# Optimization experiments

Measured on AMD Instinct MI355X. Metric: run time of the kernel, lower is better.

The kernel has to match this reference:

```python
import jax, jax.numpy as jnp
import numpy as np


def conv1x1(x, w, b):
    # x: [B,Cin,H,W], w: [Cout,Cin], b: [Cout]
    return jnp.einsum('bchw,oc->bohw', x, w) + b[None, :, None, None]


def setup_inputs() -> dict:
    key = jax.random.key(0)
    ks = jax.random.split(key, 10)
    B, Cm, C, H, W = 4, 6, 64, 64, 64
    map1 = jax.random.normal(ks[0], (B, Cm, H, W), jnp.float32)
    map2 = jax.random.normal(ks[1], (B, Cm, H, W), jnp.float32)
    feature_map = jax.random.normal(ks[2], (B, C, H, W), jnp.float32)
    # 1x1 conv params (kaiming-ish scale)
    wb = jax.random.normal(ks[3], (Cm, Cm), jnp.float32) / np.sqrt(Cm)
    bb = jnp.zeros((Cm,), jnp.float32)
    wc = jax.random.normal(ks[4], (Cm, Cm), jnp.float32) / np.sqrt(Cm)
    bc = jnp.zeros((Cm,), jnp.float32)
    wd = jax.random.normal(ks[5], (C, C), jnp.float32) / np.sqrt(C)
    bd = jnp.zeros((C,), jnp.float32)
    alpha = jnp.zeros((1,), jnp.float32)
    return {"map1": map1, "map2": map2, "feature_map": feature_map,
            "wb": wb, "bb": bb, "wc": wc, "bc": bc, "wd": wd, "bd": bd,
            "alpha": alpha}


def reference(map1, map2, feature_map, wb, bb, wc, bc, wd, bd, alpha):
    B, _, H, W = map1.shape
    N = H * W
    # conv1x1 projections, flatten spatial
    feat_b = conv1x1(map1, wb, bb).reshape(B, -1, N).transpose(0, 2, 1)  # [B,N,6]
    feat_c = conv1x1(map2, wc, bc).reshape(B, -1, N)                      # [B,6,N]
    attention_s = jax.nn.softmax(jnp.einsum('bnc,bcm->bnm', feat_b, feat_c), axis=-1)  # [B,N,N]
    feat_d = conv1x1(feature_map, wd, bd).reshape(B, -1, N)               # [B,C,N]
    # bmm with attention_s^T: out[b,c,n] = sum_m feat_d[b,c,m] * attn[b,n,m]
    feat_e = jnp.einsum('bcm,bnm->bcn', feat_d, attention_s).reshape(B, -1, H, W)
    return alpha * feat_e + feature_map
```

## Files before the change

### kernel.cpp

```cpp
#include <hip/hip_runtime.h>
#include <hip/hip_bf16.h>
#include <math.h>


#define BATCH 4
#define CMAP  6
#define CH    64
#define NSP   4096
#define TN    64
#define NTH   32
#define PSTR  72

typedef __attribute__((ext_vector_type(8))) short short8;
typedef __attribute__((ext_vector_type(4))) float f32x4;

#if __has_builtin(__builtin_amdgcn_exp2f)
#define EXP2(x) __builtin_amdgcn_exp2f(x)
#else
#define EXP2(x) exp2f(x)
#endif

__device__ __forceinline__ unsigned f2bf(float f) {
    unsigned u = __float_as_uint(f);
    return (u + 0x7fffu + ((u >> 16) & 1u)) >> 16;
}

#define INVLN2 1.44269504088896f
#define SHIFT_BF16 0xC238u
#define ONE_BF16   0x3F80u


__global__ void proj_kernel(const float* __restrict__ map1, const float* __restrict__ map2,
                            const float* __restrict__ fm,
                            const float* __restrict__ wb, const float* __restrict__ bb,
                            const float* __restrict__ wc, const float* __restrict__ bc,
                            const float* __restrict__ wd, const float* __restrict__ bd,
                            unsigned short* __restrict__ featq8,
                            unsigned short* __restrict__ featk8,
                            unsigned short* __restrict__ featdf)
{
    __shared__ unsigned short vfrag[2048];

    const int b    = blockIdx.z;
    const int half = blockIdx.y;
    const int lane = threadIdx.x & 63;
    const int og   = threadIdx.x >> 6;
    const int n    = blockIdx.x * 64 + lane;

    const int ht = lane >> 5;
    const int mm = lane & 31;
    const int q4 = mm >> 3, jj = mm & 7;
    const int cb_local = og >> 1;
    float vals[CH];
#pragma unroll
    for (int c = 0; c < CH; ++c)
        vals[c] = fm[(size_t)(b*CH + c)*NSP + n];
#pragma unroll
    for (int oi = 0; oi < 8; ++oi) {
        const int o = half*32 + og*8 + oi;
        float a = bd[o];
#pragma unroll
        for (int c = 0; c < CH; ++c)
            a = fmaf(vals[c], wd[o*CH + c], a);
        const int r = (og & 1)*8 + oi;
        vfrag[(ht*2 + cb_local)*512 + (q4*16 + r)*8 + jj] = (unsigned short)f2bf(a);
    }

    if (half == 0 && og == 0) {
        float v1[CMAP], v2[CMAP];
#pragma unroll
        for (int c = 0; c < CMAP; ++c) {
            v1[c] = map1[(size_t)(b*CMAP + c)*NSP + n];
            v2[c] = map2[(size_t)(b*CMAP + c)*NSP + n];
        }
        unsigned qv[CMAP], kv[CMAP];
#pragma unroll
        for (int o = 0; o < CMAP; ++o) {
            float a1 = bb[o], a2 = bc[o];
#pragma unroll
            for (int c = 0; c < CMAP; ++c) {
                a1 = fmaf(v1[c], wb[o*CMAP + c], a1);
                a2 = fmaf(v2[c], wc[o*CMAP + c], a2);
            }
            qv[o] = f2bf(a1 * INVLN2);
            kv[o] = f2bf(a2);
        }
        uint4 qw, kw;
        qw.x = qv[0] | (qv[1] << 16);
        qw.y = qv[2] | (qv[3] << 16);
        qw.z = qv[4] | (qv[5] << 16);
        qw.w = SHIFT_BF16;
        kw.x = kv[0] | (kv[1] << 16);
        kw.y = kv[2] | (kv[3] << 16);
        kw.z = kv[4] | (kv[5] << 16);
        kw.w = ONE_BF16;
        *(uint4*)&featq8[(size_t)(b*NSP + n)*8] = qw;
        *(uint4*)&featk8[(size_t)(b*NSP + n)*8] = kw;
    }

    __syncthreads();

    {
        const int tt = threadIdx.x;
        const uint4 d = *(const uint4*)&vfrag[tt*8];
        const int ht2 = tt >> 7, inner = tt & 127;
        const size_t off = (((size_t)(b*128 + blockIdx.x*2 + ht2)*4) + half*2)*512
                         + (size_t)inner*8;
        *(uint4*)&featdf[off] = d;
    }
}

__global__ __launch_bounds__(256, 2)
void attn_kernel(const unsigned short* __restrict__ featq8,
                 const unsigned short* __restrict__ featk8,
                 const unsigned short* __restrict__ featdf,
                 const float* __restrict__ fm, const float* __restrict__ alpha_p,
                 float* __restrict__ out)
{
    __shared__ unsigned short p_scr[2][4][16*PSTR];
    __shared__ float cmb[2][64][21];

    const int b    = blockIdx.y;
    const int t    = threadIdx.x;
    const int lane = t & 63, w = t >> 6;
    const int row16 = lane & 15, quad = lane >> 4;
    const int qsub  = w >> 1;
    const int khalf = w & 1;
    const int n0w  = blockIdx.x * 32 + qsub * 16;
    const int m0   = khalf * (NSP/2);

    short8 qf = {0,0,0,0,0,0,0,0};
    if (quad == 0)
        qf = *(const short8*)&featq8[(size_t)(b*NSP + n0w + row16)*8];

    const short8 onesb = {(short)ONE_BF16,(short)ONE_BF16,(short)ONE_BF16,(short)ONE_BF16,
                          (short)ONE_BF16,(short)ONE_BF16,(short)ONE_BF16,(short)ONE_BF16};

    const unsigned short* kbase = featk8 + ((size_t)(b*NSP + m0) + row16)*8 + quad*8;
    const unsigned short* vfb = featdf + ((size_t)b*128*4)*512 + lane*8;
    const int hb = khalf * 64;

    const f32x4 zf = {0.f,0.f,0.f,0.f};
    f32x4 acc[4] = {zf, zf, zf, zf};
    f32x4 accL = zf;
    const int prow = row16 * PSTR;

#define PAM_DO(pwp, mb, sv)                                                     \
    {                                                                           \
        const float p0 = EXP2(sv[0]), p1 = EXP2(sv[1]);                         \
        const float p2 = EXP2(sv[2]), p3 = EXP2(sv[3]);                         \
        uint2 pp;                                                               \
        pp.x = __builtin_amdgcn_perm(__float_as_uint(p1), __float_as_uint(p0), 0x07060302u); \
        pp.y = __builtin_amdgcn_perm(__float_as_uint(p3), __float_as_uint(p2), 0x07060302u); \
        *(uint2*)((pwp) + (mb)*16) = pp;                                        \
    }

#define LOADK(dst, mt)                                                          \
    dst##0 = *(const short8*)(kbase + ((mt)*TN +  0)*8);                        \
    dst##1 = *(const short8*)(kbase + ((mt)*TN + 16)*8);                        \
    dst##2 = *(const short8*)(kbase + ((mt)*TN + 32)*8);                        \
    dst##3 = *(const short8*)(kbase + ((mt)*TN + 48)*8);

#define LOADV(dst, vt)                                                          \
    dst##0 = *(const short8*)(vfb + (size_t)((hb + (vt)*2 + 0)*4 + 0)*512);     \
    dst##1 = *(const short8*)(vfb + (size_t)((hb + (vt)*2 + 1)*4 + 0)*512);     \
    dst##2 = *(const short8*)(vfb + (size_t)((hb + (vt)*2 + 0)*4 + 1)*512);     \
    dst##3 = *(const short8*)(vfb + (size_t)((hb + (vt)*2 + 1)*4 + 1)*512);     \
    dst##4 = *(const short8*)(vfb + (size_t)((hb + (vt)*2 + 0)*4 + 2)*512);     \
    dst##5 = *(const short8*)(vfb + (size_t)((hb + (vt)*2 + 1)*4 + 2)*512);     \
    dst##6 = *(const short8*)(vfb + (size_t)((hb + (vt)*2 + 0)*4 + 3)*512);     \
    dst##7 = *(const short8*)(vfb + (size_t)((hb + (vt)*2 + 1)*4 + 3)*512);

#define PV(a0_, a1_, vset)                                                      \
    acc[0] = __builtin_amdgcn_mfma_f32_16x16x32_bf16(a0_, vset##0, acc[0], 0, 0, 0); \
    acc[0] = __builtin_amdgcn_mfma_f32_16x16x32_bf16(a1_, vset##1, acc[0], 0, 0, 0); \
    acc[1] = __builtin_amdgcn_mfma_f32_16x16x32_bf16(a0_, vset##2, acc[1], 0, 0, 0); \
    acc[1] = __builtin_amdgcn_mfma_f32_16x16x32_bf16(a1_, vset##3, acc[1], 0, 0, 0); \
    acc[2] = __builtin_amdgcn_mfma_f32_16x16x32_bf16(a0_, vset##4, acc[2], 0, 0, 0); \
    acc[2] = __builtin_amdgcn_mfma_f32_16x16x32_bf16(a1_, vset##5, acc[2], 0, 0, 0); \
    acc[3] = __builtin_amdgcn_mfma_f32_16x16x32_bf16(a0_, vset##6, acc[3], 0, 0, 0); \
    acc[3] = __builtin_amdgcn_mfma_f32_16x16x32_bf16(a1_, vset##7, acc[3], 0, 0, 0); \
    accL   = __builtin_amdgcn_mfma_f32_16x16x32_bf16(a0_, onesb, accL, 0, 0, 0);     \
    accL   = __builtin_amdgcn_mfma_f32_16x16x32_bf16(a1_, onesb, accL, 0, 0, 0);

    short8 kc0, kc1, kc2, kc3, kn0, kn1, kn2, kn3;
    short8 vv0, vv1, vv2, vv3, vv4, vv5, vv6, vv7;
    short8 vn0, vn1, vn2, vn3, vn4, vn5, vn6, vn7;
    f32x4 sp0, sp1, sp2, sp3;

    LOADK(kc, 0)
    LOADV(vv, 0)
    LOADV(vn, 1)

    {
        f32x4 a0 = __builtin_amdgcn_mfma_f32_16x16x32_bf16(kc0, qf, zf, 0, 0, 0);
        f32x4 a1 = __builtin_amdgcn_mfma_f32_16x16x32_bf16(kc1, qf, zf, 0, 0, 0);
        f32x4 a2 = __builtin_amdgcn_mfma_f32_16x16x32_bf16(kc2, qf, zf, 0, 0, 0);
        f32x4 a3 = __builtin_amdgcn_mfma_f32_16x16x32_bf16(kc3, qf, zf, 0, 0, 0);
        LOADK(kc, 1)
        unsigned short* pw = &p_scr[0][w][prow + quad*4];
        PAM_DO(pw, 0, a0) PAM_DO(pw, 1, a1) PAM_DO(pw, 2, a2) PAM_DO(pw, 3, a3)
    }
    sp0 = __builtin_amdgcn_mfma_f32_16x16x32_bf16(kc0, qf, zf, 0, 0, 0);
    sp1 = __builtin_amdgcn_mfma_f32_16x16x32_bf16(kc1, qf, zf, 0, 0, 0);
    sp2 = __builtin_amdgcn_mfma_f32_16x16x32_bf16(kc2, qf, zf, 0, 0, 0);
    sp3 = __builtin_amdgcn_mfma_f32_16x16x32_bf16(kc3, qf, zf, 0, 0, 0);
    LOADK(kc, 2)

#pragma unroll 2
    for (int i = 2; i < NTH; ++i) {
        const f32x4 t0 = __builtin_amdgcn_mfma_f32_16x16x32_bf16(kc0, qf, zf, 0, 0, 0);
        const f32x4 t1 = __builtin_amdgcn_mfma_f32_16x16x32_bf16(kc1, qf, zf, 0, 0, 0);
        const f32x4 t2 = __builtin_amdgcn_mfma_f32_16x16x32_bf16(kc2, qf, zf, 0, 0, 0);
        const f32x4 t3 = __builtin_amdgcn_mfma_f32_16x16x32_bf16(kc3, qf, zf, 0, 0, 0);

        const unsigned short* pr = &p_scr[i & 1][w][prow + quad*8];
        const short8 a0 = *(const short8*)pr;
        const short8 a1 = *(const short8*)(pr + 32);

        LOADK(kn, i + 1)

        {
            unsigned short* pw = &p_scr[(i + 1) & 1][w][prow + quad*4];
            PAM_DO(pw, 0, sp0) PAM_DO(pw, 1, sp1) PAM_DO(pw, 2, sp2) PAM_DO(pw, 3, sp3)
        }

        PV(a0, a1, vv)

        vv0 = vn0; vv1 = vn1; vv2 = vn2; vv3 = vn3;
        vv4 = vn4; vv5 = vn5; vv6 = vn6; vv7 = vn7;
        LOADV(vn, i)
        kc0 = kn0; kc1 = kn1; kc2 = kn2; kc3 = kn3;
        sp0 = t0; sp1 = t1; sp2 = t2; sp3 = t3;
    }

    {
        const unsigned short* pr = &p_scr[0][w][prow + quad*8];
        const short8 a0 = *(const short8*)pr;
        const short8 a1 = *(const short8*)(pr + 32);
        unsigned short* pw = &p_scr[1][w][prow + quad*4];
        PAM_DO(pw, 0, sp0) PAM_DO(pw, 1, sp1) PAM_DO(pw, 2, sp2) PAM_DO(pw, 3, sp3)
        PV(a0, a1, vv)
        vv0 = vn0; vv1 = vn1; vv2 = vn2; vv3 = vn3;
        vv4 = vn4; vv5 = vn5; vv6 = vn6; vv7 = vn7;
    }
    {
        const unsigned short* pr = &p_scr[1][w][prow + quad*8];
        const short8 a0 = *(const short8*)pr;
        const short8 a1 = *(const short8*)(pr + 32);
        PV(a0, a1, vv)
    }
#undef PAM_DO
#undef LOADK
#undef LOADV
#undef PV

    if (khalf == 1) {
        float* c = cmb[qsub][lane];
#pragma unroll
        for (int cb = 0; cb < 4; ++cb)
            *(float4*)&c[cb*4] = (float4){acc[cb][0], acc[cb][1], acc[cb][2], acc[cb][3]};
        *(float4*)&c[16] = (float4){accL[0], accL[1], accL[2], accL[3]};
    }
    __syncthreads();
    if (khalf == 0) {
        const float* c = cmb[qsub][lane];
        const float4 lo = *(const float4*)&c[16];
        const float alpha = alpha_p[0];
        const float c0 = alpha / (accL[0] + lo.x + 1e-30f);
        const float c1 = alpha / (accL[1] + lo.y + 1e-30f);
        const float c2 = alpha / (accL[2] + lo.z + 1e-30f);
        const float c3 = alpha / (accL[3] + 1e-30f + lo.w);
#pragma unroll
        for (int cb = 0; cb < 4; ++cb) {
            const float4 po = *(const float4*)&c[cb*4];
            const int ch = cb*16 + row16;
            const size_t base = (size_t)(b*CH + ch)*NSP + n0w + quad*4;
            const float4 f = *(const float4*)&fm[base];
            float4 o;
            o.x = fmaf(c0, acc[cb][0] + po.x, f.x);
            o.y = fmaf(c1, acc[cb][1] + po.y, f.y);
            o.z = fmaf(c2, acc[cb][2] + po.z, f.z);
            o.w = fmaf(c3, acc[cb][3] + po.w, f.w);
            *(float4*)&out[base] = o;
        }
    }
}

extern "C" void kernel_launch(void* const* d_in, const int* in_sizes, int n_in,
                              void* d_out, int out_size, void* d_ws, size_t ws_size,
                              hipStream_t stream)
{
    const float* map1  = (const float*)d_in[0];
    const float* map2  = (const float*)d_in[1];
    const float* fm    = (const float*)d_in[2];
    const float* wb    = (const float*)d_in[3];
    const float* bb    = (const float*)d_in[4];
    const float* wc    = (const float*)d_in[5];
    const float* bc    = (const float*)d_in[6];
    const float* wd    = (const float*)d_in[7];
    const float* bd    = (const float*)d_in[8];
    const float* alpha = (const float*)d_in[9];
    float* out = (float*)d_out;

    unsigned short* featq8 = (unsigned short*)d_ws;
    unsigned short* featk8 = featq8 + (size_t)BATCH*NSP*8;
    unsigned short* featdf = featk8 + (size_t)BATCH*NSP*8;

    proj_kernel<<<dim3(NSP/64, 2, BATCH), 256, 0, stream>>>(
        map1, map2, fm, wb, bb, wc, bc, wd, bd, featq8, featk8, featdf);
    attn_kernel<<<dim3(NSP/32, BATCH), 256, 0, stream>>>(
        featq8, featk8, featdf, fm, alpha, out);
}
```

Before: 118.4 us.

## Split key range four ways across waves and drop register double-buffering

The attention kernel now gives each block 16 queries and has its four waves each cover a quarter of the key/value range, instead of two query sub-blocks each split into two key halves. The grid doubles, and the three partial accumulators plus row sums are combined through shared memory by wave 0. The K/V prefetch registers are removed and launch bounds raised to allow more resident blocks, trading explicit register pipelining for occupancy-based latency hiding. Each block now covers half as many queries for the same full sweep of K and V, so K/V reads through L2 roughly double.

```diff
diff --git a/kernel.cpp b/kernel.cpp
--- a/kernel.cpp
+++ b/kernel.cpp
@@ -8,7 +8,7 @@
 #define CH    64
 #define NSP   4096
 #define TN    64
-#define NTH   32
+#define NTW   16
 #define PSTR  72
 
 typedef __attribute__((ext_vector_type(8))) short short8;
@@ -110,7 +110,7 @@
     }
 }
 
-__global__ __launch_bounds__(256, 2)
+__global__ __launch_bounds__(256, 4)
 void attn_kernel(const unsigned short* __restrict__ featq8,
                  const unsigned short* __restrict__ featk8,
                  const unsigned short* __restrict__ featdf,
@@ -118,27 +118,25 @@
                  float* __restrict__ out)
 {
     __shared__ unsigned short p_scr[2][4][16*PSTR];
-    __shared__ float cmb[2][64][21];
+    __shared__ float cmb[3][64][20];
 
     const int b    = blockIdx.y;
     const int t    = threadIdx.x;
     const int lane = t & 63, w = t >> 6;
     const int row16 = lane & 15, quad = lane >> 4;
-    const int qsub  = w >> 1;
-    const int khalf = w & 1;
-    const int n0w  = blockIdx.x * 32 + qsub * 16;
-    const int m0   = khalf * (NSP/2);
+    const int n0   = blockIdx.x * 16;
+    const int m0   = w * (NSP/4);
 
     short8 qf = {0,0,0,0,0,0,0,0};
     if (quad == 0)
-        qf = *(const short8*)&featq8[(size_t)(b*NSP + n0w + row16)*8];
+        qf = *(const short8*)&featq8[(size_t)(b*NSP + n0 + row16)*8];
 
     const short8 onesb = {(short)ONE_BF16,(short)ONE_BF16,(short)ONE_BF16,(short)ONE_BF16,
                           (short)ONE_BF16,(short)ONE_BF16,(short)ONE_BF16,(short)ONE_BF16};
 
     const unsigned short* kbase = featk8 + ((size_t)(b*NSP + m0) + row16)*8 + quad*8;
     const unsigned short* vfb = featdf + ((size_t)b*128*4)*512 + lane*8;
-    const int hb = khalf * 64;
+    const int hb = w * 32;
 
     const f32x4 zf = {0.f,0.f,0.f,0.f};
     f32x4 acc[4] = {zf, zf, zf, zf};
@@ -155,49 +153,45 @@
         *(uint2*)((pwp) + (mb)*16) = pp;                                        \
     }
 
-#define LOADK(dst, mt)                                                          \
-    dst##0 = *(const short8*)(kbase + ((mt)*TN +  0)*8);                        \
-    dst##1 = *(const short8*)(kbase + ((mt)*TN + 16)*8);                        \
-    dst##2 = *(const short8*)(kbase + ((mt)*TN + 32)*8);                        \
-    dst##3 = *(const short8*)(kbase + ((mt)*TN + 48)*8);
-
-#define LOADV(dst, vt)                                                          \
-    dst##0 = *(const short8*)(vfb + (size_t)((hb + (vt)*2 + 0)*4 + 0)*512);     \
-    dst##1 = *(const short8*)(vfb + (size_t)((hb + (vt)*2 + 1)*4 + 0)*512);     \
-    dst##2 = *(const short8*)(vfb + (size_t)((hb + (vt)*2 + 0)*4 + 1)*512);     \
-    dst##3 = *(const short8*)(vfb + (size_t)((hb + (vt)*2 + 1)*4 + 1)*512);     \
-    dst##4 = *(const short8*)(vfb + (size_t)((hb + (vt)*2 + 0)*4 + 2)*512);     \
-    dst##5 = *(const short8*)(vfb + (size_t)((hb + (vt)*2 + 1)*4 + 2)*512);     \
-    dst##6 = *(const short8*)(vfb + (size_t)((hb + (vt)*2 + 0)*4 + 3)*512);     \
-    dst##7 = *(const short8*)(vfb + (size_t)((hb + (vt)*2 + 1)*4 + 3)*512);
-
-#define PV(a0_, a1_, vset)                                                      \
-    acc[0] = __builtin_amdgcn_mfma_f32_16x16x32_bf16(a0_, vset##0, acc[0], 0, 0, 0); \
-    acc[0] = __builtin_amdgcn_mfma_f32_16x16x32_bf16(a1_, vset##1, acc[0], 0, 0, 0); \
-    acc[1] = __builtin_amdgcn_mfma_f32_16x16x32_bf16(a0_, vset##2, acc[1], 0, 0, 0); \
-    acc[1] = __builtin_amdgcn_mfma_f32_16x16x32_bf16(a1_, vset##3, acc[1], 0, 0, 0); \
-    acc[2] = __builtin_amdgcn_mfma_f32_16x16x32_bf16(a0_, vset##4, acc[2], 0, 0, 0); \
-    acc[2] = __builtin_amdgcn_mfma_f32_16x16x32_bf16(a1_, vset##5, acc[2], 0, 0, 0); \
-    acc[3] = __builtin_amdgcn_mfma_f32_16x16x32_bf16(a0_, vset##6, acc[3], 0, 0, 0); \
-    acc[3] = __builtin_amdgcn_mfma_f32_16x16x32_bf16(a1_, vset##7, acc[3], 0, 0, 0); \
-    accL   = __builtin_amdgcn_mfma_f32_16x16x32_bf16(a0_, onesb, accL, 0, 0, 0);     \
+#define LOADK(mt)                                                               \
+    kc0 = *(const short8*)(kbase + ((mt)*TN +  0)*8);                           \
+    kc1 = *(const short8*)(kbase + ((mt)*TN + 16)*8);                           \
+    kc2 = *(const short8*)(kbase + ((mt)*TN + 32)*8);                           \
+    kc3 = *(const short8*)(kbase + ((mt)*TN + 48)*8);
+
+#define LOADV(vt)                                                               \
+    vv0 = *(const short8*)(vfb + (size_t)((hb + (vt)*2 + 0)*4 + 0)*512);        \
+    vv1 = *(const short8*)(vfb + (size_t)((hb + (vt)*2 + 1)*4 + 0)*512);        \
+    vv2 = *(const short8*)(vfb + (size_t)((hb + (vt)*2 + 0)*4 + 1)*512);        \
+    vv3 = *(const short8*)(vfb + (size_t)((hb + (vt)*2 + 1)*4 + 1)*512);        \
+    vv4 = *(const short8*)(vfb + (size_t)((hb + (vt)*2 + 0)*4 + 2)*512);        \
+    vv5 = *(const short8*)(vfb + (size_t)((hb + (vt)*2 + 1)*4 + 2)*512);        \
+    vv6 = *(const short8*)(vfb + (size_t)((hb + (vt)*2 + 1)*4 + 3)*512);        \
+    vv7 = *(const short8*)(vfb + (size_t)((hb + (vt)*2 + 0)*4 + 3)*512);
+
+#define PV(a0_, a1_)                                                            \
+    acc[0] = __builtin_amdgcn_mfma_f32_16x16x32_bf16(a0_, vv0, acc[0], 0, 0, 0); \
+    acc[0] = __builtin_amdgcn_mfma_f32_16x16x32_bf16(a1_, vv1, acc[0], 0, 0, 0); \
+    acc[1] = __builtin_amdgcn_mfma_f32_16x16x32_bf16(a0_, vv2, acc[1], 0, 0, 0); \
+    acc[1] = __builtin_amdgcn_mfma_f32_16x16x32_bf16(a1_, vv3, acc[1], 0, 0, 0); \
+    acc[2] = __builtin_amdgcn_mfma_f32_16x16x32_bf16(a0_, vv4, acc[2], 0, 0, 0); \
+    acc[2] = __builtin_amdgcn_mfma_f32_16x16x32_bf16(a1_, vv5, acc[2], 0, 0, 0); \
+    acc[3] = __builtin_amdgcn_mfma_f32_16x16x32_bf16(a0_, vv7, acc[3], 0, 0, 0); \
+    acc[3] = __builtin_amdgcn_mfma_f32_16x16x32_bf16(a1_, vv6, acc[3], 0, 0, 0); \
+    accL   = __builtin_amdgcn_mfma_f32_16x16x32_bf16(a0_, onesb, accL, 0, 0, 0); \
     accL   = __builtin_amdgcn_mfma_f32_16x16x32_bf16(a1_, onesb, accL, 0, 0, 0);
 
-    short8 kc0, kc1, kc2, kc3, kn0, kn1, kn2, kn3;
+    short8 kc0, kc1, kc2, kc3;
     short8 vv0, vv1, vv2, vv3, vv4, vv5, vv6, vv7;
-    short8 vn0, vn1, vn2, vn3, vn4, vn5, vn6, vn7;
     f32x4 sp0, sp1, sp2, sp3;
 
-    LOADK(kc, 0)
-    LOADV(vv, 0)
-    LOADV(vn, 1)
-
+    LOADK(0)
     {
         f32x4 a0 = __builtin_amdgcn_mfma_f32_16x16x32_bf16(kc0, qf, zf, 0, 0, 0);
         f32x4 a1 = __builtin_amdgcn_mfma_f32_16x16x32_bf16(kc1, qf, zf, 0, 0, 0);
         f32x4 a2 = __builtin_amdgcn_mfma_f32_16x16x32_bf16(kc2, qf, zf, 0, 0, 0);
         f32x4 a3 = __builtin_amdgcn_mfma_f32_16x16x32_bf16(kc3, qf, zf, 0, 0, 0);
-        LOADK(kc, 1)
+        LOADK(1)
         unsigned short* pw = &p_scr[0][w][prow + quad*4];
         PAM_DO(pw, 0, a0) PAM_DO(pw, 1, a1) PAM_DO(pw, 2, a2) PAM_DO(pw, 3, a3)
     }
@@ -205,32 +199,31 @@
     sp1 = __builtin_amdgcn_mfma_f32_16x16x32_bf16(kc1, qf, zf, 0, 0, 0);
     sp2 = __builtin_amdgcn_mfma_f32_16x16x32_bf16(kc2, qf, zf, 0, 0, 0);
     sp3 = __builtin_amdgcn_mfma_f32_16x16x32_bf16(kc3, qf, zf, 0, 0, 0);
-    LOADK(kc, 2)
+    LOADK(2)
+    LOADV(0)
 
 #pragma unroll 2
-    for (int i = 2; i < NTH; ++i) {
+    for (int i = 2; i < NTW; ++i) {
         const f32x4 t0 = __builtin_amdgcn_mfma_f32_16x16x32_bf16(kc0, qf, zf, 0, 0, 0);
         const f32x4 t1 = __builtin_amdgcn_mfma_f32_16x16x32_bf16(kc1, qf, zf, 0, 0, 0);
         const f32x4 t2 = __builtin_amdgcn_mfma_f32_16x16x32_bf16(kc2, qf, zf, 0, 0, 0);
         const f32x4 t3 = __builtin_amdgcn_mfma_f32_16x16x32_bf16(kc3, qf, zf, 0, 0, 0);
 
+        LOADK(i + 1)
+
         const unsigned short* pr = &p_scr[i & 1][w][prow + quad*8];
         const short8 a0 = *(const short8*)pr;
         const short8 a1 = *(const short8*)(pr + 32);
 
-        LOADK(kn, i + 1)
-
         {
             unsigned short* pw = &p_scr[(i + 1) & 1][w][prow + quad*4];
             PAM_DO(pw, 0, sp0) PAM_DO(pw, 1, sp1) PAM_DO(pw, 2, sp2) PAM_DO(pw, 3, sp3)
         }
 
-        PV(a0, a1, vv)
-
-        vv0 = vn0; vv1 = vn1; vv2 = vn2; vv3 = vn3;
-        vv4 = vn4; vv5 = vn5; vv6 = vn6; vv7 = vn7;
-        LOADV(vn, i)
-        kc0 = kn0; kc1 = kn1; kc2 = kn2; kc3 = kn3;
+        PV(a0, a1)
+
+        LOADV(i - 1)
+
         sp0 = t0; sp1 = t1; sp2 = t2; sp3 = t3;
     }
 
@@ -240,48 +233,56 @@
         const short8 a1 = *(const short8*)(pr + 32);
         unsigned short* pw = &p_scr[1][w][prow + quad*4];
         PAM_DO(pw, 0, sp0) PAM_DO(pw, 1, sp1) PAM_DO(pw, 2, sp2) PAM_DO(pw, 3, sp3)
-        PV(a0, a1, vv)
-        vv0 = vn0; vv1 = vn1; vv2 = vn2; vv3 = vn3;
-        vv4 = vn4; vv5 = vn5; vv6 = vn6; vv7 = vn7;
+        PV(a0, a1)
+        LOADV(15)
     }
     {
         const unsigned short* pr = &p_scr[1][w][prow + quad*8];
         const short8 a0 = *(const short8*)pr;
         const short8 a1 = *(const short8*)(pr + 32);
-        PV(a0, a1, vv)
+        PV(a0, a1)
     }
 #undef PAM_DO
 #undef LOADK
 #undef LOADV
 #undef PV
 
-    if (khalf == 1) {
-        float* c = cmb[qsub][lane];
+    if (w != 0) {
+        float* c = cmb[w - 1][lane];
 #pragma unroll
         for (int cb = 0; cb < 4; ++cb)
             *(float4*)&c[cb*4] = (float4){acc[cb][0], acc[cb][1], acc[cb][2], acc[cb][3]};
         *(float4*)&c[16] = (float4){accL[0], accL[1], accL[2], accL[3]};
     }
     __syncthreads();
-    if (khalf == 0) {
-        const float* c = cmb[qsub][lane];
-        const float4 lo = *(const float4*)&c[16];
+    if (w == 0) {
+#pragma unroll
+        for (int ww = 0; ww < 3; ++ww) {
+            const float* c = cmb[ww][lane];
+#pragma unroll
+            for (int cb = 0; cb < 4; ++cb) {
+                const float4 po = *(const float4*)&c[cb*4];
+                acc[cb][0] += po.x; acc[cb][1] += po.y;
+                acc[cb][2] += po.z; acc[cb][3] += po.w;
+            }
+            const float4 lo = *(const float4*)&c[16];
+            accL[0] += lo.x; accL[1] += lo.y; accL[2] += lo.z; accL[3] += lo.w;
+        }
         const float alpha = alpha_p[0];
-        const float c0 = alpha / (accL[0] + lo.x + 1e-30f);
-        const float c1 = alpha / (accL[1] + lo.y + 1e-30f);
-        const float c2 = alpha / (accL[2] + lo.z + 1e-30f);
-        const float c3 = alpha / (accL[3] + 1e-30f + lo.w);
+        const float c0 = alpha / (accL[0] + 1e-30f);
+        const float c1 = alpha / (accL[1] + 1e-30f);
+        const float c2 = alpha / (accL[2] + 1e-30f);
+        const float c3 = alpha / (accL[3] + 1e-30f);
 #pragma unroll
         for (int cb = 0; cb < 4; ++cb) {
-            const float4 po = *(const float4*)&c[cb*4];
             const int ch = cb*16 + row16;
-            const size_t base = (size_t)(b*CH + ch)*NSP + n0w + quad*4;
+            const size_t base = (size_t)(b*CH + ch)*NSP + n0 + quad*4;
             const float4 f = *(const float4*)&fm[base];
             float4 o;
-            o.x = fmaf(c0, acc[cb][0] + po.x, f.x);
-            o.y = fmaf(c1, acc[cb][1] + po.y, f.y);
-            o.z = fmaf(c2, acc[cb][2] + po.z, f.z);
-            o.w = fmaf(c3, acc[cb][3] + po.w, f.w);
+            o.x = fmaf(c0, acc[cb][0], f.x);
+            o.y = fmaf(c1, acc[cb][1], f.y);
+            o.z = fmaf(c2, acc[cb][2], f.z);
+            o.w = fmaf(c3, acc[cb][3], f.w);
             *(float4*)&out[base] = o;
         }
     }
@@ -309,6 +310,6 @@
 
     proj_kernel<<<dim3(NSP/64, 2, BATCH), 256, 0, stream>>>(
         map1, map2, fm, wb, bb, wc, bc, wd, bd, featq8, featk8, featdf);
-    attn_kernel<<<dim3(NSP/32, BATCH), 256, 0, stream>>>(
+    attn_kernel<<<dim3(NSP/16, BATCH), 256, 0, stream>>>(
         featq8, featk8, featdf, fm, alpha, out);
 }
```

After: 122.1 us. 3.1% more time.
